# Performance work log

Measured on AMD Instinct MI355X. Metric: run time of the kernel, lower is better.

Reference implementation:

```python
import jax, jax.numpy as jnp
import numpy as np

N = 10000; E = 320000
DIM = 176; ATT = 16; SH_HEADS = 16; TH = 4; NH = SH_HEADS + TH; VD = DIM // SH_HEADS
LMAX = 3; NSPH = (LMAX + 1) ** 2; ZDIM = 16; RDIM = 16
RSTART = 0.8; CUT = 5.0; NLAYERS = 2


def _ln(x):
    mu = jnp.mean(x, axis=-1, keepdims=True)
    dx = x - mu
    var = jnp.mean(dx ** 2, axis=-1, keepdims=True)
    return dx * (1e-6 + var) ** (-0.5)


def _sph(v):
    # real spherical harmonics up to l=3, unnormalized overall scale, [E,16]
    x, y, z = v[..., 0], v[..., 1], v[..., 2]
    s3 = np.float32(np.sqrt(3.0)); s15 = np.float32(np.sqrt(15.0))
    c1 = np.float32(np.sqrt(5.0 / 8.0)); c2 = np.float32(np.sqrt(3.0 / 8.0))
    x2, y2, z2 = x * x, y * y, z * z
    return jnp.stack([
        jnp.ones_like(x),
        x, y, z,
        s3 * x * y, s3 * y * z, 0.5 * (3.0 * z2 - 1.0), s3 * x * z, 0.5 * s3 * (x2 - y2),
        c1 * y * (3.0 * x2 - y2), s15 * x * y * z, c2 * y * (5.0 * z2 - 1.0),
        0.5 * z * (5.0 * z2 - 3.0), c2 * x * (5.0 * z2 - 1.0),
        0.5 * s15 * z * (x2 - y2), c1 * x * (x2 - 3.0 * y2),
    ], axis=-1)


def setup_inputs() -> dict:
    key = jax.random.key(0)
    ks = jax.random.split(key, 32)

    def rn(k, shape):
        fan_in = shape[0] if len(shape) > 1 else shape[0]
        return jax.random.normal(k, shape, dtype=jnp.float32) / np.float32(np.sqrt(shape[0]))

    species = jax.random.randint(ks[0], (N,), 0, 64)
    edge_src = jax.random.randint(ks[1], (E,), 0, N)
    edge_dst = jax.random.randint(ks[2], (E,), 0, N)
    distances = RSTART + (CUT - RSTART) * jax.random.uniform(ks[3], (E,), dtype=jnp.float32)
    raw = jax.random.normal(ks[4], (E, 3), dtype=jnp.float32)
    dirn = raw / jnp.linalg.norm(raw, axis=-1, keepdims=True)
    vec = dirn * distances[:, None]
    switch = 0.5 * (jnp.cos(jnp.pi * distances / CUT) + 1.0)

    inp = {
        'species': species, 'distances': distances, 'switch': switch,
        'edge_src': edge_src, 'edge_dst': edge_dst, 'vec': vec,
        'z_table': jax.random.normal(ks[5], (64, ZDIM), dtype=jnp.float32),
        'w_species': rn(ks[6], (ZDIM, DIM)),
        'pos_w1_0': rn(ks[7], (RDIM, 2 * ATT)), 'pos_b1_0': jnp.zeros((2 * ATT,), jnp.float32),
        'pos_w2_0': rn(ks[8], (2 * ATT, ATT)), 'pos_b2_0': jnp.zeros((ATT,), jnp.float32),
        'wq_0': rn(ks[9], (DIM, NH * ATT)), 'wk_0': rn(ks[10], (DIM, NH * ATT)),
        'wv_0': rn(ks[11], (DIM, SH_HEADS * VD)),
        'upd_w_0': rn(ks[12], (2 * DIM, DIM)), 'upd_b_0': jnp.zeros((DIM,), jnp.float32),
        'pos_w1_1': rn(ks[13], (RDIM + TH * (LMAX + 1), 2 * ATT)), 'pos_b1_1': jnp.zeros((2 * ATT,), jnp.float32),
        'pos_w2_1': rn(ks[14], (2 * ATT, ATT)), 'pos_b2_1': jnp.zeros((ATT,), jnp.float32),
        'wq_1': rn(ks[15], (DIM, NH * ATT)), 'wk_1': rn(ks[16], (DIM, NH * ATT)),
        'wv_1': rn(ks[17], (DIM, SH_HEADS * VD)),
        'upd_w_1': rn(ks[18], (2 * DIM, DIM)), 'upd_b_1': jnp.zeros((DIM,), jnp.float32),
    }
    return inp


def reference(species, distances, switch, edge_src, edge_dst, vec,
              z_table, w_species,
              pos_w1_0, pos_b1_0, pos_w2_0, pos_b2_0, wq_0, wk_0, wv_0, upd_w_0, upd_b_0,
              pos_w1_1, pos_b1_1, pos_w2_1, pos_b2_1, wq_1, wk_1, wv_1, upd_w_1, upd_b_1):
    Nn = species.shape[0]
    Zi = z_table[species]                      # [N, ZDIM] species encoding
    xi = _ln(Zi @ w_species)                   # [N, DIM]

    vhat = vec / distances[:, None]
    Yij = _sph(vhat)                           # [E, NSPH]
    ls = np.repeat(np.arange(LMAX + 1), 2 * np.arange(LMAX + 1) + 1)
    parity = jnp.asarray(((-1.0) ** ls).astype(np.float32))  # [NSPH]

    centers = jnp.linspace(RSTART, CUT, RDIM, dtype=jnp.float32)
    sigma = np.float32((CUT - RSTART) / (RDIM - 1))
    radial = jnp.exp(-(((distances[:, None] - centers) / sigma) ** 2))  # [E, RDIM]

    Vi = jnp.zeros((Nn, TH, NSPH), jnp.float32)
    pos = [(pos_w1_0, pos_b1_0, pos_w2_0, pos_b2_0), (pos_w1_1, pos_b1_1, pos_w2_1, pos_b2_1)]
    att = [(wq_0, wk_0, wv_0, upd_w_0, upd_b_0), (wq_1, wk_1, wv_1, upd_w_1, upd_b_1)]
    inv_sqrt_d = np.float32(1.0 / np.sqrt(ATT))

    for layer in range(NLAYERS):
        pw1, pb1, pw2, pb2 = pos[layer]
        wq, wk, wv, uw, ub = att[layer]
        if layer == 0:
            ur = radial
        else:
            # tensor relative positional features: [E, TH, NSPH]
            xij2 = (Vi[edge_dst] + (parity * Vi)[edge_src]) * Yij[:, None, :]
            us = [xij2[:, :, l * l:(l + 1) * (l + 1)].sum(axis=-1) for l in range(LMAX + 1)]
            ur = jnp.concatenate([radial] + us, axis=-1)
        w = jax.nn.swish(ur @ pw1 + pb1) @ pw2 + pb2     # [E, ATT] positional encoding
        q = (xi @ wq).reshape(Nn, NH, ATT)
        k = (xi @ wk).reshape(Nn, NH, ATT)
        # multiplicative relative positional attention coefficients [E, NH]
        aij = jnp.einsum('ehd,ed->eh', q[edge_dst] * k[edge_src], w) * (switch[:, None] * inv_sqrt_d)
        a_s, a_t = aij[:, :SH_HEADS], aij[:, SH_HEADS:]
        v = (xi @ wv).reshape(Nn, SH_HEADS, VD)
        mi = jax.ops.segment_sum(a_s[:, :, None] * v[edge_src], edge_dst, num_segments=Nn)  # [N,SH,VD]
        Vi = Vi + jax.ops.segment_sum(
            a_t[:, :, None] * (Yij[:, None, :] + parity * Vi[edge_src]), edge_dst, num_segments=Nn)
        ui = jnp.concatenate([xi, mi.reshape(Nn, -1)], axis=-1)
        xi = _ln(xi + ui @ uw + ub)
    return xi
```

## Files before the change

### kernel.cpp

```cpp
#include <hip/hip_runtime.h>
#include <hip/hip_bf16.h>
#include <math.h>

#define N_NODES 10000
#define N_PAD   10048
#define N_EDGES 320000
#define DIM     176
#define ATT     16
#define SH_HEADS 16
#define THH     4
#define NH      20
#define VD      11
#define ZDIM    16
#define RDIM    16
#define QK_W    (NH*ATT)
#define QKV_W   816
#define UI_W    (2*DIM)
#define KQ      192
#define SIGINV  3.5714285714285716f
#define RSTEP   0.28f

typedef unsigned short ushort_t;
typedef __attribute__((ext_vector_type(8))) short bf16x8;
typedef __attribute__((ext_vector_type(4))) float f32x4;


__device__ __forceinline__ ushort_t f2bf(float f) {
    __hip_bfloat16 b = __float2bfloat16(f);
    return *(ushort_t*)&b;
}

__device__ __forceinline__ float bf2f(ushort_t u) {
    return __uint_as_float(((unsigned)u) << 16);
}

__device__ __forceinline__ void sph16(float x, float y, float z, float* Y) {
    const float s3  = 1.7320508075688772f;
    const float s15 = 3.872983346207417f;
    const float c1  = 0.7905694150420949f;
    const float c2  = 0.6123724356957945f;
    float x2 = x*x, y2 = y*y, z2 = z*z;
    Y[0]  = 1.0f;
    Y[1]  = x;
    Y[2]  = y;
    Y[3]  = z;
    Y[4]  = s3 * x * y;
    Y[5]  = s3 * y * z;
    Y[6]  = 0.5f * (3.0f * z2 - 1.0f);
    Y[7]  = s3 * x * z;
    Y[8]  = 0.5f * s3 * (x2 - y2);
    Y[9]  = c1 * y * (3.0f * x2 - y2);
    Y[10] = s15 * x * y * z;
    Y[11] = c2 * y * (5.0f * z2 - 1.0f);
    Y[12] = 0.5f * z * (5.0f * z2 - 3.0f);
    Y[13] = c2 * x * (5.0f * z2 - 1.0f);
    Y[14] = 0.5f * s15 * z * (x2 - y2);
    Y[15] = c1 * x * (x2 - 3.0f * y2);
}

__device__ __forceinline__ void unpack8(const uint4 u, float* f) {
    f[0] = __uint_as_float(u.x << 16);
    f[1] = __uint_as_float(u.x & 0xffff0000u);
    f[2] = __uint_as_float(u.y << 16);
    f[3] = __uint_as_float(u.y & 0xffff0000u);
    f[4] = __uint_as_float(u.z << 16);
    f[5] = __uint_as_float(u.z & 0xffff0000u);
    f[6] = __uint_as_float(u.w << 16);
    f[7] = __uint_as_float(u.w & 0xffff0000u);
}


__device__ __forceinline__ void deg_body(int bid, int tid,
        const int* __restrict__ edst, const int* __restrict__ esrc,
        const float* __restrict__ dist, const float* __restrict__ swit,
        const float* __restrict__ vec, int* deg, int* rank, uint4* pk) {
    int e = bid * 256 + tid;
    if (e >= N_EDGES) return;
    int t_ = edst[e];
    rank[e] = atomicAdd(&deg[t_], 1);
    uint4 a, b;
    a.x = (unsigned)esrc[e];
    a.y = (unsigned)t_;
    a.z = __float_as_uint(dist[e]);
    a.w = __float_as_uint(swit[e]);
    b.x = __float_as_uint(vec[(size_t)e*3 + 0]);
    b.y = __float_as_uint(vec[(size_t)e*3 + 1]);
    b.z = __float_as_uint(vec[(size_t)e*3 + 2]);
    b.w = 0u;
    pk[(size_t)e*2 + 0] = a;
    pk[(size_t)e*2 + 1] = b;
}

__device__ __forceinline__ void prep_qkv_body(int bid, int tid, const float* wq,
        const float* wk, const float* wv, ushort_t* Wtq) {
    int id = bid * 256 + tid;
    if (id >= 832 * KQ) return;
    int n = id / KQ, k = id - (id / KQ) * KQ;
    float v = 0.0f;
    if (k < DIM && n < QKV_W)
        v = (n < 320) ? wq[k * 320 + n] : (n < 640) ? wk[k * 320 + (n - 320)]
                                                    : wv[k * DIM + (n - 640)];
    Wtq[id] = f2bf(v);
}

__device__ __forceinline__ void prep_upd_body(int bid, int tid, const float* uw, ushort_t* Wtu) {
    int id = bid * 256 + tid;
    if (id >= 192 * UI_W) return;
    int n = id / UI_W, k = id - (id / UI_W) * UI_W;
    float v = (n < DIM) ? uw[k * DIM + n] : 0.0f;
    Wtu[id] = f2bf(v);
}

__device__ __forceinline__ void prep_mlp_body(int bid, int tid, const float* pw1,
        const float* pw2, ushort_t* w1T, ushort_t* w2T, int K1) {
    int id = bid * 256 + tid;
    if (id < 1024) {
        int n = id >> 5, k = id & 31;
        w1T[n * 32 + k] = (k < K1) ? f2bf(pw1[k * 32 + n]) : 0;
    } else if (id < 1536) {
        int id2 = id - 1024;
        int n = id2 >> 5, k = id2 & 31;
        w2T[n * 32 + k] = f2bf(pw2[k * 16 + n]);
    }
}

struct InitSmem {
    float zs[16 * ZDIM];
    float yt[16 * DIM];
    float red[256];
    float mus[16], rstds[16];
};

__device__ void init_body(int bid, int tid, InitSmem& sm,
        const int* species, const float* z_table, const float* wsp,
        float* xi, ushort_t* xib, ushort_t* cxm) {
    int base = bid * 16;
    { int n = tid >> 4, kk = tid & 15;
      sm.zs[tid] = z_table[species[base + n] * ZDIM + kk]; }
    __syncthreads();
    int c = tid;
    if (c < DIM) {
        float acc[16];
        #pragma unroll
        for (int n = 0; n < 16; n++) acc[n] = 0.0f;
        for (int kk = 0; kk < ZDIM; kk++) {
            float w = wsp[kk * DIM + c];
            #pragma unroll
            for (int n = 0; n < 16; n++) acc[n] += sm.zs[n * ZDIM + kk] * w;
        }
        #pragma unroll
        for (int n = 0; n < 16; n++) sm.yt[n * DIM + c] = acc[n];
    }
    __syncthreads();
    { int n2 = tid >> 4, j = tid & 15;
      float s = 0.0f;
      for (int c2 = j; c2 < DIM; c2 += 16) s += sm.yt[n2 * DIM + c2];
      sm.red[tid] = s; }
    __syncthreads();
    if (tid < 16) { float s = 0; for (int j = 0; j < 16; j++) s += sm.red[tid * 16 + j]; sm.mus[tid] = s / (float)DIM; }
    __syncthreads();
    { int n2 = tid >> 4, j = tid & 15;
      float mu = sm.mus[n2], s = 0.0f;
      for (int c2 = j; c2 < DIM; c2 += 16) { float d = sm.yt[n2 * DIM + c2] - mu; s += d * d; }
      sm.red[tid] = s; }
    __syncthreads();
    if (tid < 16) { float s = 0; for (int j = 0; j < 16; j++) s += sm.red[tid * 16 + j]; sm.rstds[tid] = rsqrtf(s / (float)DIM + 1e-6f); }
    __syncthreads();
    if (c < DIM) {
        #pragma unroll
        for (int n = 0; n < 16; n++) {
            float val = (sm.yt[n * DIM + c] - sm.mus[n]) * sm.rstds[n];
            xi[(size_t)(base + n) * DIM + c] = val;
            ushort_t bv = f2bf(val);
            xib[(size_t)(base + n) * KQ + c]   = bv;
            cxm[(size_t)(base + n) * UI_W + c] = bv;
        }
    } else if (c < KQ) {
        #pragma unroll
        for (int n = 0; n < 16; n++) xib[(size_t)(base + n) * KQ + c] = 0;
    }
}

__global__ __launch_bounds__(256) void k_pre(
        const int* edst, const int* esrc, const float* dist, const float* swit,
        const float* vec, int* deg, int* rank, uint4* pk,
        const float* wq0, const float* wk0, const float* wv0, ushort_t* Wtq0,
        const float* wq1, const float* wk1, const float* wv1, ushort_t* Wtq1,
        const float* uw0, ushort_t* Wtu0, const float* uw1, ushort_t* Wtu1,
        const float* pw1_0, const float* pw2_0, ushort_t* w1T0, ushort_t* w2T0,
        const float* pw1_1, const float* pw2_1, ushort_t* w1T1, ushort_t* w2T1,
        const int* species, const float* z_table, const float* wsp,
        float* xi, ushort_t* xib, ushort_t* cxm) {
    __shared__ InitSmem sm;
    int bid = blockIdx.x, tid = threadIdx.x;
    if (bid < 1250)       deg_body(bid, tid, edst, esrc, dist, swit, vec, deg, rank, pk);
    else if (bid < 1874)  prep_qkv_body(bid - 1250, tid, wq0, wk0, wv0, Wtq0);
    else if (bid < 2498)  prep_qkv_body(bid - 1874, tid, wq1, wk1, wv1, Wtq1);
    else if (bid < 2762)  prep_upd_body(bid - 2498, tid, uw0, Wtu0);
    else if (bid < 3026)  prep_upd_body(bid - 2762, tid, uw1, Wtu1);
    else if (bid < 3032)  prep_mlp_body(bid - 3026, tid, pw1_0, pw2_0, w1T0, w2T0, 16);
    else if (bid < 3038)  prep_mlp_body(bid - 3032, tid, pw1_1, pw2_1, w1T1, w2T1, 32);
    else                  init_body(bid - 3038, tid, sm, species, z_table, wsp, xi, xib, cxm);
}


__global__ __launch_bounds__(1024) void k_scan(const int* __restrict__ deg, int* off) {
    __shared__ int sd[1024];
    int tid = threadIdx.x;
    int base = tid * 10;
    int v[10];
    int s = 0;
    #pragma unroll
    for (int j = 0; j < 10; j++) {
        int gi = base + j;
        v[j] = (gi < N_NODES) ? deg[gi] : 0;
        s += v[j];
    }
    sd[tid] = s;
    __syncthreads();
    for (int st = 1; st < 1024; st <<= 1) {
        int add = (tid >= st) ? sd[tid - st] : 0;
        __syncthreads();
        sd[tid] += add;
        __syncthreads();
    }
    int run = (tid > 0) ? sd[tid - 1] : 0;
    #pragma unroll
    for (int j = 0; j < 10; j++) {
        run += v[j];
        int gi = base + j;
        if (gi < N_NODES) off[gi + 1] = run;
    }
    if (tid == 0) off[0] = 0;
}

__global__ __launch_bounds__(256) void k_perm(const int* edst, const int* rank,
                                              const int* off, int* perm) {
    int e = blockIdx.x * 256 + threadIdx.x;
    if (e >= N_EDGES) return;
    perm[off[edst[e]] + rank[e]] = e;
}

__global__ __launch_bounds__(256) void k_build(const int* __restrict__ perm,
        const uint4* __restrict__ pk,
        int* src_c, int* dst_c, float* dist_c, float* sc_c, float* Yf) {
    int p = blockIdx.x * 256 + threadIdx.x;
    if (p >= N_EDGES) return;
    int e  = perm[p];
    uint4 a = pk[(size_t)e*2 + 0];
    uint4 b = pk[(size_t)e*2 + 1];
    int s  = (int)a.x;
    int t_ = (int)a.y;
    float d  = __uint_as_float(a.z);
    float sw = __uint_as_float(a.w);
    float inv = 1.0f / d;
    float vx = __uint_as_float(b.x) * inv;
    float vy = __uint_as_float(b.y) * inv;
    float vz = __uint_as_float(b.z) * inv;
    src_c[p]  = s;
    dst_c[p]  = t_;
    dist_c[p] = d;
    sc_c[p]   = sw * 0.25f;
    float Y[16];
    sph16(vx, vy, vz, Y);
    #pragma unroll
    for (int m = 0; m < 16; m += 4)
        *(float4*)&Yf[(size_t)p * 16 + m] = make_float4(Y[m], Y[m+1], Y[m+2], Y[m+3]);
}


__global__ __launch_bounds__(256) void k_gemmq(const ushort_t* __restrict__ A,
                                               const ushort_t* __restrict__ Bt,
                                               ushort_t* __restrict__ qh,
                                               ushort_t* __restrict__ kh,
                                               ushort_t* __restrict__ vh) {
    __shared__ ushort_t As[64 * 200];
    __shared__ ushort_t Bs[64 * 200];
    int tid  = threadIdx.x;
    int m0   = blockIdx.y * 64, n0 = blockIdx.x * 64;
    int w    = tid >> 6, lane = tid & 63, quad = lane >> 4, c16 = lane & 15;
    #pragma unroll
    for (int it = 0; it < 6; it++) {
        int seg = it * 256 + tid;
        int r = seg / 24, cs = seg - (seg / 24) * 24;
        *(uint4*)&As[r * 200 + cs * 8] =
            *(const uint4*)&A[(size_t)(m0 + r) * KQ + cs * 8];
        *(uint4*)&Bs[r * 200 + cs * 8] =
            *(const uint4*)&Bt[(size_t)(n0 + r) * KQ + cs * 8];
    }
    __syncthreads();
    f32x4 acc[4] = {};
    #pragma unroll
    for (int kc = 0; kc < 6; kc++) {
        bf16x8 a = *(const bf16x8*)&As[(w * 16 + c16) * 200 + kc * 32 + quad * 8];
        #pragma unroll
        for (int t = 0; t < 4; t++) {
            bf16x8 b = *(const bf16x8*)&Bs[(t * 16 + c16) * 200 + kc * 32 + quad * 8];
            acc[t] = __builtin_amdgcn_mfma_f32_16x16x32_bf16(a, b, acc[t], 0, 0, 0);
        }
    }
    #pragma unroll
    for (int t = 0; t < 4; t++) {
        #pragma unroll
        for (int r = 0; r < 4; r++) {
            int row = m0 + w * 16 + quad * 4 + r;
            int col = n0 + t * 16 + c16;
            if (row < N_NODES && col < QKV_W) {
                ushort_t bv = f2bf(acc[t][r]);
                if (col < 320)      qh[(size_t)row * QK_W + col] = bv;
                else if (col < 640) kh[(size_t)row * QK_W + (col - 320)] = bv;
                else                vh[(size_t)row * DIM  + (col - 640)] = bv;
            }
        }
    }
}


__global__ __launch_bounds__(256) void k_updln(const ushort_t* __restrict__ A,
        const ushort_t* __restrict__ Bt, const float* __restrict__ xi,
        const float* __restrict__ ub,
        float* xo, ushort_t* xib, ushort_t* cxm) {
    __shared__ ushort_t As[64 * 360];
    int tid  = threadIdx.x;
    int m0   = blockIdx.x * 64;
    int w    = tid >> 6, lane = tid & 63, quad = lane >> 4, c16 = lane & 15;
    #pragma unroll
    for (int it = 0; it < 11; it++) {
        int seg = it * 256 + tid;
        int r = seg / 44, cs = seg - (seg / 44) * 44;
        *(uint4*)&As[r * 360 + cs * 8] =
            *(const uint4*)&A[(size_t)(m0 + r) * UI_W + cs * 8];
    }
    __syncthreads();
    f32x4 acc[11] = {};
    for (int kc = 0; kc < 11; kc++) {
        bf16x8 a = *(const bf16x8*)&As[(w * 16 + c16) * 360 + kc * 32 + quad * 8];
        #pragma unroll
        for (int t = 0; t < 11; t++) {
            bf16x8 b = *(const bf16x8*)&Bt[(size_t)(t * 16 + c16) * UI_W + kc * 32 + quad * 8];
            acc[t] = __builtin_amdgcn_mfma_f32_16x16x32_bf16(a, b, acc[t], 0, 0, 0);
        }
    }
    float ubv[11];
    #pragma unroll
    for (int t = 0; t < 11; t++) ubv[t] = ub[t * 16 + c16];
    int rowb = m0 + w * 16 + quad * 4;
    #pragma unroll
    for (int r = 0; r < 4; r++) {
        int row = rowb + r;
        if (row >= N_NODES) continue;
        float srow = 0.0f;
        #pragma unroll
        for (int t = 0; t < 11; t++) {
            float val = acc[t][r] + xi[(size_t)row * DIM + t * 16 + c16] + ubv[t];
            acc[t][r] = val;
            srow += val;
        }
        srow += __shfl_xor(srow, 1);
        srow += __shfl_xor(srow, 2);
        srow += __shfl_xor(srow, 4);
        srow += __shfl_xor(srow, 8);
        float mu = srow / (float)DIM;
        float sv = 0.0f;
        #pragma unroll
        for (int t = 0; t < 11; t++) { float d = acc[t][r] - mu; sv += d * d; }
        sv += __shfl_xor(sv, 1);
        sv += __shfl_xor(sv, 2);
        sv += __shfl_xor(sv, 4);
        sv += __shfl_xor(sv, 8);
        float rstd = rsqrtf(sv / (float)DIM + 1e-6f);
        #pragma unroll
        for (int t = 0; t < 11; t++) {
            int col = t * 16 + c16;
            float nv = (acc[t][r] - mu) * rstd;
            xo[(size_t)row * DIM + col] = nv;
            ushort_t bv = f2bf(nv);
            xib[(size_t)row * KQ + col]   = bv;
            cxm[(size_t)row * UI_W + col] = bv;
        }
    }
}


template<bool L0>
__global__ __launch_bounds__(256) void k_edge(const float* dist_c, const float* sc_c,
        const int* src_c, const int* dst_c, const float* Yf, const ushort_t* Vih,
        const ushort_t* qh, const ushort_t* kh,
        const ushort_t* w1T, const float* pb1, const ushort_t* w2T, const float* pb2,
        ushort_t* aijh) {
    __shared__ ushort_t urS[64 * 40];
    __shared__ ushort_t Ht[4][16 * 40];
    __shared__ float    wdS[64 * 17];
    __shared__ ushort_t aS[NH][64];
    int tid  = threadIdx.x;
    int w    = tid >> 6, lane = tid & 63, quad = lane >> 4, c16 = lane & 15;
    int eb   = blockIdx.x * 64;

    int le = tid >> 2, part = tid & 3;
    int ie = eb + le;
    int sE = src_c[ie], tE = dst_c[ie];

    if (!L0) {
        int e  = tid & 63, tp = tid >> 6;
        int i  = eb + e;
        float d = dist_c[i];
        ushort_t ur4[4];
        #pragma unroll
        for (int r0 = 0; r0 < 4; r0++) {
            int r = tp * 4 + r0;
            float cc = 0.8f + (float)r * RSTEP;
            float uu = (d - cc) * SIGINV;
            ur4[r0] = f2bf(__expf(-uu * uu));
        }
        *(uint2*)&urS[e * 40 + tp * 4] = *(uint2*)ur4;
        float Y[16];
        #pragma unroll
        for (int m = 0; m < 16; m += 4) {
            float4 y = *(const float4*)&Yf[(size_t)i * 16 + m];
            Y[m] = y.x; Y[m+1] = y.y; Y[m+2] = y.z; Y[m+3] = y.w;
        }
        int s = src_c[i], t_ = dst_c[i];
        const uint4* vd4 = (const uint4*)(Vih + (size_t)t_ * 64);
        const uint4* vs4 = (const uint4*)(Vih + (size_t)s  * 64);
        int th = tp;
        float fd[16], fs[16];
        unpack8(vd4[2*th],   fd);     unpack8(vd4[2*th+1], fd+8);
        unpack8(vs4[2*th],   fs);     unpack8(vs4[2*th+1], fs+8);
        float us0 = (fd[0] + fs[0]) * Y[0];
        float us1 = 0.0f, us2 = 0.0f, us3 = 0.0f;
        #pragma unroll
        for (int m = 1; m < 4; m++)  us1 += (fd[m] - fs[m]) * Y[m];
        #pragma unroll
        for (int m = 4; m < 9; m++)  us2 += (fd[m] + fs[m]) * Y[m];
        #pragma unroll
        for (int m = 9; m < 16; m++) us3 += (fd[m] - fs[m]) * Y[m];
        urS[e * 40 + 16 + 0 * 4 + th] = f2bf(us0);
        urS[e * 40 + 16 + 1 * 4 + th] = f2bf(us1);
        urS[e * 40 + 16 + 2 * 4 + th] = f2bf(us2);
        urS[e * 40 + 16 + 3 * 4 + th] = f2bf(us3);
        __syncthreads();
    }

    uint4 kr[10];
    {
        const uint4* kseg = (const uint4*)(kh + (size_t)sE * QK_W) + part * 10;
        #pragma unroll
        for (int j = 0; j < 10; j++) kr[j] = kseg[j];
    }

    {
        int e0 = eb + w * 16;
        bf16x8 a1;
        if (L0) {
            float d = dist_c[e0 + c16];
            #pragma unroll
            for (int j = 0; j < 8; j++) {
                int r = quad * 8 + j;
                float v = 0.0f;
                if (r < 16) { float cc = 0.8f + (float)r * RSTEP; float uu = (d - cc) * SIGINV; v = __expf(-uu * uu); }
                a1[j] = (short)f2bf(v);
            }
        } else {
            a1 = *(const bf16x8*)&urS[(w * 16 + c16) * 40 + quad * 8];
        }
        bf16x8 b0 = *(const bf16x8*)&w1T[c16 * 32 + quad * 8];
        bf16x8 b1 = *(const bf16x8*)&w1T[(16 + c16) * 32 + quad * 8];
        f32x4 acc0 = {}, acc1 = {};
        acc0 = __builtin_amdgcn_mfma_f32_16x16x32_bf16(a1, b0, acc0, 0, 0, 0);
        acc1 = __builtin_amdgcn_mfma_f32_16x16x32_bf16(a1, b1, acc1, 0, 0, 0);
        float bb0 = pb1[c16], bb1 = pb1[c16 + 16];
        #pragma unroll
        for (int r = 0; r < 4; r++) {
            int er = quad * 4 + r;
            float h0 = acc0[r] + bb0; h0 = h0 / (1.0f + __expf(-h0));
            float h1 = acc1[r] + bb1; h1 = h1 / (1.0f + __expf(-h1));
            Ht[w][er * 40 + c16]      = f2bf(h0);
            Ht[w][er * 40 + 16 + c16] = f2bf(h1);
        }
        __syncthreads();
        bf16x8 a2 = *(const bf16x8*)&Ht[w][c16 * 40 + quad * 8];
        bf16x8 b2 = *(const bf16x8*)&w2T[c16 * 32 + quad * 8];
        f32x4 acc2 = {};
        acc2 = __builtin_amdgcn_mfma_f32_16x16x32_bf16(a2, b2, acc2, 0, 0, 0);
        float bb2 = pb2[c16];
        #pragma unroll
        for (int r = 0; r < 4; r++) {
            int er = quad * 4 + r;
            wdS[(w * 16 + er) * 17 + c16] = (acc2[r] + bb2) * sc_c[e0 + er];
        }
    }
    __syncthreads();

    {
        float wd[16];
        #pragma unroll
        for (int p = 0; p < 16; p++) wd[p] = wdS[le * 17 + p];
        const uint4* q4 = (const uint4*)(qh + (size_t)tE * QK_W) + part * 10;
        #pragma unroll
        for (int j = 0; j < 5; j++) {
            int h = part * 5 + j;
            float qa[8], qb[8], ka[8], kb[8];
            unpack8(q4[2*j],   qa); unpack8(q4[2*j+1], qb);
            unpack8(kr[2*j],   ka); unpack8(kr[2*j+1], kb);
            float acc = 0.0f;
            #pragma unroll
            for (int dd = 0; dd < 8; dd++) acc += qa[dd] * ka[dd] * wd[dd];
            #pragma unroll
            for (int dd = 0; dd < 8; dd++) acc += qb[dd] * kb[dd] * wd[8 + dd];
            aS[h][le] = f2bf(acc);
        }
    }
    __syncthreads();
    {
        const uint* aSw = (const uint*)aS;
        for (int idx = tid; idx < NH * 32; idx += 256) {
            int h = idx >> 5, w2 = idx & 31;
            *(uint*)(aijh + (size_t)h * N_EDGES + eb + w2 * 2) = aSw[h * 32 + w2];
        }
    }
}


__device__ __forceinline__ void mi_step(int i, int c0, bool f1, bool f2,
        const int* src_c, const ushort_t* aA, const ushort_t* aB, const ushort_t* vh,
        float& acc0, float& acc1, float& acc2, float& acc3) {
    int s0 = src_c[i];
    uint2 v0 = *(const uint2*)(vh + (size_t)s0 * DIM + c0);
    float a00 = bf2f(aA[i]), a0B = bf2f(aB[i]);
    float g01 = f1 ? a0B : a00, g02 = f2 ? a0B : a00;
    acc0 += a00 * __uint_as_float(v0.x << 16);
    acc1 += g01 * __uint_as_float(v0.x & 0xffff0000u);
    acc2 += g02 * __uint_as_float(v0.y << 16);
    acc3 += a0B * __uint_as_float(v0.y & 0xffff0000u);
}

__device__ __forceinline__ void mi_wave(int n, int lane, const int* off, const int* src_c,
        const ushort_t* aijh, const ushort_t* vh, ushort_t* cxm) {
    if (lane >= 44) return;
    int c0 = lane * 4;
    int hA = c0 / VD;
    int hB = (c0 + 3) / VD;
    bool f1 = ((c0 + 1) / VD) != hA;
    bool f2 = ((c0 + 2) / VD) != hA;
    const ushort_t* aA = aijh + (size_t)hA * N_EDGES;
    const ushort_t* aB = aijh + (size_t)hB * N_EDGES;
    int start = off[n], end = off[n + 1];
    float acc0 = 0, acc1 = 0, acc2 = 0, acc3 = 0;
    int cnt = end - start;
    int i = start;

#define MI_ACC(vv, av, bv) { \
    float aa = bf2f(av), ab = bf2f(bv); \
    float g1 = f1 ? ab : aa, g2 = f2 ? ab : aa; \
    acc0 += aa * __uint_as_float((vv).x << 16); \
    acc1 += g1 * __uint_as_float((vv).x & 0xffff0000u); \
    acc2 += g2 * __uint_as_float((vv).y << 16); \
    acc3 += ab * __uint_as_float((vv).y & 0xffff0000u); }

    if (cnt >= 4) {
        int iend = start + (cnt & ~3);
        int s0 = src_c[i], s1 = src_c[i+1], s2 = src_c[i+2], s3 = src_c[i+3];
        uint2 v0 = *(const uint2*)(vh + (size_t)s0 * DIM + c0);
        uint2 v1 = *(const uint2*)(vh + (size_t)s1 * DIM + c0);
        uint2 v2 = *(const uint2*)(vh + (size_t)s2 * DIM + c0);
        uint2 v3 = *(const uint2*)(vh + (size_t)s3 * DIM + c0);
        ushort_t pA0 = aA[i], pA1 = aA[i+1], pA2 = aA[i+2], pA3 = aA[i+3];
        ushort_t pB0 = aB[i], pB1 = aB[i+1], pB2 = aB[i+2], pB3 = aB[i+3];
        for (i += 4; i + 4 <= iend; i += 4) {
            int t0 = src_c[i], t1 = src_c[i+1], t2 = src_c[i+2], t3 = src_c[i+3];
            uint2 w0 = *(const uint2*)(vh + (size_t)t0 * DIM + c0);
            uint2 w1 = *(const uint2*)(vh + (size_t)t1 * DIM + c0);
            uint2 w2 = *(const uint2*)(vh + (size_t)t2 * DIM + c0);
            uint2 w3 = *(const uint2*)(vh + (size_t)t3 * DIM + c0);
            ushort_t qA0 = aA[i], qA1 = aA[i+1], qA2 = aA[i+2], qA3 = aA[i+3];
            ushort_t qB0 = aB[i], qB1 = aB[i+1], qB2 = aB[i+2], qB3 = aB[i+3];
            MI_ACC(v0, pA0, pB0); MI_ACC(v1, pA1, pB1);
            MI_ACC(v2, pA2, pB2); MI_ACC(v3, pA3, pB3);
            v0 = w0; v1 = w1; v2 = w2; v3 = w3;
            pA0 = qA0; pA1 = qA1; pA2 = qA2; pA3 = qA3;
            pB0 = qB0; pB1 = qB1; pB2 = qB2; pB3 = qB3;
        }
        MI_ACC(v0, pA0, pB0); MI_ACC(v1, pA1, pB1);
        MI_ACC(v2, pA2, pB2); MI_ACC(v3, pA3, pB3);
    }
    for (; i < end; i++)
        mi_step(i, c0, f1, f2, src_c, aA, aB, vh, acc0, acc1, acc2, acc3);
#undef MI_ACC
    ushort_t o[4] = {f2bf(acc0), f2bf(acc1), f2bf(acc2), f2bf(acc3)};
    *(uint2*)(cxm + (size_t)n * UI_W + DIM + c0) = *(uint2*)o;
}

__device__ __forceinline__ void vi_wave(int n, int lane, const int* off,
        const float* Yf, const ushort_t* aijh, ushort_t* Vih) {
    int th = lane >> 4, sm = lane & 15;
    const ushort_t* ah = aijh + (size_t)(SH_HEADS + th) * N_EDGES;
    int start = off[n], end = off[n + 1];
    float acc = 0.0f;
    int cnt = end - start;
    int i = start;
    if (cnt >= 4) {
        int iend = start + (cnt & ~3);
        float a0 = bf2f(ah[i]),   y0 = Yf[(size_t)i * 16 + sm];
        float a1 = bf2f(ah[i+1]), y1 = Yf[(size_t)(i+1) * 16 + sm];
        float a2 = bf2f(ah[i+2]), y2 = Yf[(size_t)(i+2) * 16 + sm];
        float a3 = bf2f(ah[i+3]), y3 = Yf[(size_t)(i+3) * 16 + sm];
        for (i += 4; i + 4 <= iend; i += 4) {
            float b0 = bf2f(ah[i]),   z0 = Yf[(size_t)i * 16 + sm];
            float b1 = bf2f(ah[i+1]), z1 = Yf[(size_t)(i+1) * 16 + sm];
            float b2 = bf2f(ah[i+2]), z2 = Yf[(size_t)(i+2) * 16 + sm];
            float b3 = bf2f(ah[i+3]), z3 = Yf[(size_t)(i+3) * 16 + sm];
            acc += a0 * y0 + a1 * y1 + a2 * y2 + a3 * y3;
            a0 = b0; a1 = b1; a2 = b2; a3 = b3;
            y0 = z0; y1 = z1; y2 = z2; y3 = z3;
        }
        acc += a0 * y0 + a1 * y1 + a2 * y2 + a3 * y3;
    }
    for (; i < end; i++)
        acc += bf2f(ah[i]) * Yf[(size_t)i * 16 + sm];
    Vih[(size_t)n * 64 + lane] = f2bf(acc);
}

__global__ __launch_bounds__(256) void k_agg0(const int* off, const int* src_c,
        const float* Yf, const ushort_t* aijh, const ushort_t* vh,
        ushort_t* cxm, ushort_t* Vih) {
    int wid  = blockIdx.x * 4 + (threadIdx.x >> 6);
    int lane = threadIdx.x & 63;
    if (wid < N_NODES)
        mi_wave(wid, lane, off, src_c, aijh, vh, cxm);
    else
        vi_wave(wid - N_NODES, lane, off, Yf, aijh, Vih);
}

__global__ __launch_bounds__(256) void k_agg1(const int* off, const int* src_c,
        const ushort_t* aijh, const ushort_t* vh, ushort_t* cxm) {
    int wid  = blockIdx.x * 4 + (threadIdx.x >> 6);
    int lane = threadIdx.x & 63;
    mi_wave(wid, lane, off, src_c, aijh, vh, cxm);
}


extern "C" void kernel_launch(void* const* d_in, const int* in_sizes, int n_in,
                              void* d_out, int out_size, void* d_ws, size_t ws_size,
                              hipStream_t stream) {
    const int*   species = (const int*)  d_in[0];
    const float* dist    = (const float*)d_in[1];
    const float* swit    = (const float*)d_in[2];
    const int*   esrc    = (const int*)  d_in[3];
    const int*   edst    = (const int*)  d_in[4];
    const float* vec     = (const float*)d_in[5];
    const float* z_table = (const float*)d_in[6];
    const float* wsp     = (const float*)d_in[7];
    const float* pw1_0 = (const float*)d_in[8],  *pb1_0 = (const float*)d_in[9];
    const float* pw2_0 = (const float*)d_in[10], *pb2_0 = (const float*)d_in[11];
    const float* wq0 = (const float*)d_in[12], *wk0 = (const float*)d_in[13];
    const float* wv0 = (const float*)d_in[14], *uw0 = (const float*)d_in[15];
    const float* ub0 = (const float*)d_in[16];
    const float* pw1_1 = (const float*)d_in[17], *pb1_1 = (const float*)d_in[18];
    const float* pw2_1 = (const float*)d_in[19], *pb2_1 = (const float*)d_in[20];
    const float* wq1 = (const float*)d_in[21], *wk1 = (const float*)d_in[22];
    const float* wv1 = (const float*)d_in[23], *uw1 = (const float*)d_in[24];
    const float* ub1 = (const float*)d_in[25];
    float* out = (float*)d_out;

    char* p = (char*)d_ws;
    auto alloc = [&](size_t bytes) -> char* {
        char* r = p;
        p += (bytes + 255) & ~(size_t)255;
        return r;
    };
    int* deg    = (int*)alloc((size_t)N_NODES * 4);
    int* off    = (int*)alloc((size_t)(N_NODES + 1) * 4);
    int* rank   = (int*)alloc((size_t)N_EDGES * 4);
    int* perm   = (int*)alloc((size_t)N_EDGES * 4);
    uint4* pk   = (uint4*)alloc((size_t)N_EDGES * 32);
    int*   src_c  = (int*)  alloc((size_t)N_EDGES * 4);
    int*   dst_c  = (int*)  alloc((size_t)N_EDGES * 4);
    float* dist_c = (float*)alloc((size_t)N_EDGES * 4);
    float* sc_c   = (float*)alloc((size_t)N_EDGES * 4);
    float* Yf     = (float*)alloc((size_t)N_EDGES * 16 * 4);
    float* xiA  = (float*)alloc((size_t)N_NODES * DIM * 4);
    float* xiB  = (float*)alloc((size_t)N_NODES * DIM * 4);
    ushort_t* xib  = (ushort_t*)alloc((size_t)N_PAD * KQ * 2);
    ushort_t* cxm  = (ushort_t*)alloc((size_t)N_PAD * UI_W * 2);
    ushort_t* qh   = (ushort_t*)alloc((size_t)N_NODES * QK_W * 2);
    ushort_t* kh   = (ushort_t*)alloc((size_t)N_NODES * QK_W * 2);
    ushort_t* vh   = (ushort_t*)alloc((size_t)N_NODES * DIM * 2);
    ushort_t* Wtq0 = (ushort_t*)alloc((size_t)832 * KQ * 2);
    ushort_t* Wtq1 = (ushort_t*)alloc((size_t)832 * KQ * 2);
    ushort_t* Wtu0 = (ushort_t*)alloc((size_t)192 * UI_W * 2);
    ushort_t* Wtu1 = (ushort_t*)alloc((size_t)192 * UI_W * 2);
    ushort_t* w1T0 = (ushort_t*)alloc((size_t)32 * 32 * 2);
    ushort_t* w2T0 = (ushort_t*)alloc((size_t)16 * 32 * 2);
    ushort_t* w1T1 = (ushort_t*)alloc((size_t)32 * 32 * 2);
    ushort_t* w2T1 = (ushort_t*)alloc((size_t)16 * 32 * 2);
    ushort_t* Vih  = (ushort_t*)alloc((size_t)N_NODES * 64 * 2);
    ushort_t* aijh = (ushort_t*)alloc((size_t)N_EDGES * NH * 2);

    const int NB_E  = (N_EDGES + 255) / 256;
    const int NB_F  = N_EDGES / 64;
    const dim3 GRID_QKV(13, 157);

    hipMemsetAsync(deg, 0, (size_t)N_NODES * 4, stream);
    k_pre<<<3663, 256, 0, stream>>>(edst, esrc, dist, swit, vec, deg, rank, pk,
                                    wq0, wk0, wv0, Wtq0, wq1, wk1, wv1, Wtq1,
                                    uw0, Wtu0, uw1, Wtu1,
                                    pw1_0, pw2_0, w1T0, w2T0,
                                    pw1_1, pw2_1, w1T1, w2T1,
                                    species, z_table, wsp, xiA, xib, cxm);
    k_scan<<<1, 1024, 0, stream>>>(deg, off);
    k_perm<<<NB_E, 256, 0, stream>>>(edst, rank, off, perm);
    k_build<<<NB_E, 256, 0, stream>>>(perm, pk, src_c, dst_c, dist_c, sc_c, Yf);

    k_gemmq<<<GRID_QKV, 256, 0, stream>>>(xib, Wtq0, qh, kh, vh);
    k_edge<true><<<NB_F, 256, 0, stream>>>(dist_c, sc_c, src_c, dst_c, Yf, Vih,
                                           qh, kh, w1T0, pb1_0, w2T0, pb2_0, aijh);
    k_agg0<<<5000, 256, 0, stream>>>(off, src_c, Yf, aijh, vh, cxm, Vih);
    k_updln<<<157, 256, 0, stream>>>(cxm, Wtu0, xiA, ub0, xiB, xib, cxm);

    k_gemmq<<<GRID_QKV, 256, 0, stream>>>(xib, Wtq1, qh, kh, vh);
    k_edge<false><<<NB_F, 256, 0, stream>>>(dist_c, sc_c, src_c, dst_c, Yf, Vih,
                                            qh, kh, w1T1, pb1_1, w2T1, pb2_1, aijh);
    k_agg1<<<2500, 256, 0, stream>>>(off, src_c, aijh, vh, cxm);
    k_updln<<<157, 256, 0, stream>>>(cxm, Wtu1, xiB, ub1, out, xib, cxm);
}
```

Baseline: 388.4 us.

## Split update GEMM and layernorm into tiled GEMM plus separate LN kernel

```diff
diff --git a/kernel.cpp b/kernel.cpp
--- a/kernel.cpp
+++ b/kernel.cpp
@@ -316,67 +316,62 @@
 }
 
 
-__global__ __launch_bounds__(256) void k_updln(const ushort_t* __restrict__ A,
-        const ushort_t* __restrict__ Bt, const float* __restrict__ xi,
-        const float* __restrict__ ub,
-        float* xo, ushort_t* xib, ushort_t* cxm) {
-    __shared__ ushort_t As[64 * 360];
+__global__ __launch_bounds__(256) void k_gemmu(const ushort_t* __restrict__ A,
+                                               const ushort_t* __restrict__ Bt,
+                                               float* __restrict__ Cv) {
+    __shared__ ushort_t As[64 * 200];
+    __shared__ ushort_t Bs[64 * 200];
     int tid  = threadIdx.x;
-    int m0   = blockIdx.x * 64;
+    int m0   = blockIdx.y * 64, n0 = blockIdx.x * 64;
     int w    = tid >> 6, lane = tid & 63, quad = lane >> 4, c16 = lane & 15;
-    #pragma unroll
-    for (int it = 0; it < 11; it++) {
+    f32x4 acc[4] = {};
+    #pragma unroll
+    for (int it = 0; it < 6; it++) {
         int seg = it * 256 + tid;
-        int r = seg / 44, cs = seg - (seg / 44) * 44;
-        *(uint4*)&As[r * 360 + cs * 8] =
+        int r = seg / 24, cs = seg - (seg / 24) * 24;
+        *(uint4*)&As[r * 200 + cs * 8] =
             *(const uint4*)&A[(size_t)(m0 + r) * UI_W + cs * 8];
-    }
-    __syncthreads();
-    f32x4 acc[11] = {};
-    for (int kc = 0; kc < 11; kc++) {
-        bf16x8 a = *(const bf16x8*)&As[(w * 16 + c16) * 360 + kc * 32 + quad * 8];
-        #pragma unroll
-        for (int t = 0; t < 11; t++) {
-            bf16x8 b = *(const bf16x8*)&Bt[(size_t)(t * 16 + c16) * UI_W + kc * 32 + quad * 8];
+        *(uint4*)&Bs[r * 200 + cs * 8] =
+            *(const uint4*)&Bt[(size_t)(n0 + r) * UI_W + cs * 8];
+    }
+    __syncthreads();
+    #pragma unroll
+    for (int kc = 0; kc < 6; kc++) {
+        bf16x8 a = *(const bf16x8*)&As[(w * 16 + c16) * 200 + kc * 32 + quad * 8];
+        #pragma unroll
+        for (int t = 0; t < 4; t++) {
+            bf16x8 b = *(const bf16x8*)&Bs[(t * 16 + c16) * 200 + kc * 32 + quad * 8];
             acc[t] = __builtin_amdgcn_mfma_f32_16x16x32_bf16(a, b, acc[t], 0, 0, 0);
         }
     }
-    float ubv[11];
-    #pragma unroll
-    for (int t = 0; t < 11; t++) ubv[t] = ub[t * 16 + c16];
-    int rowb = m0 + w * 16 + quad * 4;
-    #pragma unroll
-    for (int r = 0; r < 4; r++) {
-        int row = rowb + r;
-        if (row >= N_NODES) continue;
-        float srow = 0.0f;
-        #pragma unroll
-        for (int t = 0; t < 11; t++) {
-            float val = acc[t][r] + xi[(size_t)row * DIM + t * 16 + c16] + ubv[t];
-            acc[t][r] = val;
-            srow += val;
-        }
-        srow += __shfl_xor(srow, 1);
-        srow += __shfl_xor(srow, 2);
-        srow += __shfl_xor(srow, 4);
-        srow += __shfl_xor(srow, 8);
-        float mu = srow / (float)DIM;
-        float sv = 0.0f;
-        #pragma unroll
-        for (int t = 0; t < 11; t++) { float d = acc[t][r] - mu; sv += d * d; }
-        sv += __shfl_xor(sv, 1);
-        sv += __shfl_xor(sv, 2);
-        sv += __shfl_xor(sv, 4);
-        sv += __shfl_xor(sv, 8);
-        float rstd = rsqrtf(sv / (float)DIM + 1e-6f);
-        #pragma unroll
-        for (int t = 0; t < 11; t++) {
-            int col = t * 16 + c16;
-            float nv = (acc[t][r] - mu) * rstd;
-            xo[(size_t)row * DIM + col] = nv;
-            ushort_t bv = f2bf(nv);
-            xib[(size_t)row * KQ + col]   = bv;
-            cxm[(size_t)row * UI_W + col] = bv;
+    __syncthreads();
+    #pragma unroll
+    for (int it = 0; it < 5; it++) {
+        int seg = it * 256 + tid;
+        int r = seg / 20, cs = seg - (seg / 20) * 20;
+        *(uint4*)&As[r * 200 + cs * 8] =
+            *(const uint4*)&A[(size_t)(m0 + r) * UI_W + 192 + cs * 8];
+        *(uint4*)&Bs[r * 200 + cs * 8] =
+            *(const uint4*)&Bt[(size_t)(n0 + r) * UI_W + 192 + cs * 8];
+    }
+    __syncthreads();
+    #pragma unroll
+    for (int kc = 0; kc < 5; kc++) {
+        bf16x8 a = *(const bf16x8*)&As[(w * 16 + c16) * 200 + kc * 32 + quad * 8];
+        #pragma unroll
+        for (int t = 0; t < 4; t++) {
+            bf16x8 b = *(const bf16x8*)&Bs[(t * 16 + c16) * 200 + kc * 32 + quad * 8];
+            acc[t] = __builtin_amdgcn_mfma_f32_16x16x32_bf16(a, b, acc[t], 0, 0, 0);
+        }
+    }
+    #pragma unroll
+    for (int t = 0; t < 4; t++) {
+        #pragma unroll
+        for (int r = 0; r < 4; r++) {
+            int row = m0 + w * 16 + quad * 4 + r;
+            int col = n0 + t * 16 + c16;
+            if (row < N_NODES && col < DIM)
+                Cv[(size_t)row * DIM + col] = acc[t][r];
         }
     }
 }
@@ -636,6 +631,50 @@
     int wid  = blockIdx.x * 4 + (threadIdx.x >> 6);
     int lane = threadIdx.x & 63;
     mi_wave(wid, lane, off, src_c, aijh, vh, cxm);
+}
+
+
+__global__ __launch_bounds__(256) void k_lnfinal(const float* yg, const float* xi,
+        const float* ub, float* xo, ushort_t* xib, ushort_t* cxm) {
+    __shared__ float yt[16 * DIM];
+    __shared__ float red[256];
+    __shared__ float mus[16], rstds[16];
+    int base = blockIdx.x * 16;
+    int tid  = threadIdx.x;
+    for (int idx = tid; idx < 16 * DIM; idx += 256) {
+        int n = idx / DIM, c = idx - n * DIM;
+        yt[idx] = xi[(size_t)(base + n) * DIM + c]
+                + yg[(size_t)(base + n) * DIM + c] + ub[c];
+    }
+    __syncthreads();
+    { int n2 = tid >> 4, j = tid & 15;
+      float s = 0.0f;
+      for (int c2 = j; c2 < DIM; c2 += 16) s += yt[n2 * DIM + c2];
+      red[tid] = s; }
+    __syncthreads();
+    if (tid < 16) { float s = 0; for (int j = 0; j < 16; j++) s += red[tid * 16 + j]; mus[tid] = s / (float)DIM; }
+    __syncthreads();
+    { int n2 = tid >> 4, j = tid & 15;
+      float mu = mus[n2], s = 0.0f;
+      for (int c2 = j; c2 < DIM; c2 += 16) { float d = yt[n2 * DIM + c2] - mu; s += d * d; }
+      red[tid] = s; }
+    __syncthreads();
+    if (tid < 16) { float s = 0; for (int j = 0; j < 16; j++) s += red[tid * 16 + j]; rstds[tid] = rsqrtf(s / (float)DIM + 1e-6f); }
+    __syncthreads();
+    int c = tid;
+    if (c < DIM) {
+        #pragma unroll
+        for (int n = 0; n < 16; n++) {
+            float val = (yt[n * DIM + c] - mus[n]) * rstds[n];
+            xo[(size_t)(base + n) * DIM + c] = val;
+            ushort_t bv = f2bf(val);
+            xib[(size_t)(base + n) * KQ + c]   = bv;
+            cxm[(size_t)(base + n) * UI_W + c] = bv;
+        }
+    } else if (c < KQ) {
+        #pragma unroll
+        for (int n = 0; n < 16; n++) xib[(size_t)(base + n) * KQ + c] = 0;
+    }
 }
 
 
@@ -685,6 +724,7 @@
     ushort_t* qh   = (ushort_t*)alloc((size_t)N_NODES * QK_W * 2);
     ushort_t* kh   = (ushort_t*)alloc((size_t)N_NODES * QK_W * 2);
     ushort_t* vh   = (ushort_t*)alloc((size_t)N_NODES * DIM * 2);
+    float* ybuf    = (float*)alloc((size_t)N_NODES * DIM * 4);
     ushort_t* Wtq0 = (ushort_t*)alloc((size_t)832 * KQ * 2);
     ushort_t* Wtq1 = (ushort_t*)alloc((size_t)832 * KQ * 2);
     ushort_t* Wtu0 = (ushort_t*)alloc((size_t)192 * UI_W * 2);
@@ -698,7 +738,9 @@
 
     const int NB_E  = (N_EDGES + 255) / 256;
     const int NB_F  = N_EDGES / 64;
+    const int NB_T  = N_NODES / 16;
     const dim3 GRID_QKV(13, 157);
+    const dim3 GRID_UPD(3, 157);
 
     hipMemsetAsync(deg, 0, (size_t)N_NODES * 4, stream);
     k_pre<<<3663, 256, 0, stream>>>(edst, esrc, dist, swit, vec, deg, rank, pk,
@@ -715,11 +757,13 @@
     k_edge<true><<<NB_F, 256, 0, stream>>>(dist_c, sc_c, src_c, dst_c, Yf, Vih,
                                            qh, kh, w1T0, pb1_0, w2T0, pb2_0, aijh);
     k_agg0<<<5000, 256, 0, stream>>>(off, src_c, Yf, aijh, vh, cxm, Vih);
-    k_updln<<<157, 256, 0, stream>>>(cxm, Wtu0, xiA, ub0, xiB, xib, cxm);
+    k_gemmu<<<GRID_UPD, 256, 0, stream>>>(cxm, Wtu0, ybuf);
+    k_lnfinal<<<NB_T, 256, 0, stream>>>(ybuf, xiA, ub0, xiB, xib, cxm);
 
     k_gemmq<<<GRID_QKV, 256, 0, stream>>>(xib, Wtq1, qh, kh, vh);
     k_edge<false><<<NB_F, 256, 0, stream>>>(dist_c, sc_c, src_c, dst_c, Yf, Vih,
                                             qh, kh, w1T1, pb1_1, w2T1, pb2_1, aijh);
     k_agg1<<<2500, 256, 0, stream>>>(off, src_c, aijh, vh, cxm);
-    k_updln<<<157, 256, 0, stream>>>(cxm, Wtu1, xiB, ub1, out, xib, cxm);
-}
+    k_gemmu<<<GRID_UPD, 256, 0, stream>>>(cxm, Wtu1, ybuf);
+    k_lnfinal<<<NB_T, 256, 0, stream>>>(ybuf, xiB, ub1, out, xib, cxm);
+}
```

After: 368.0 us. 5.3% less time.
